# Performance work log

Hardware: AMD Instinct MI355X
Metric: run time of the kernel (lower is better)

## Reference

```python
import jax, jax.numpy as jnp
from jax import lax
import numpy as np

B, N, XS, LAT = 16, 400000, 256, 10


def setup_inputs() -> dict:
    key = jax.random.key(0)
    ks = jax.random.split(key, 9)
    flow = 2.0 * jax.random.normal(ks[0], (B, N, 3), jnp.float32)
    x = jax.random.normal(ks[1], (B, XS, XS), jnp.float32)
    values = jax.random.normal(ks[2], (N,), jnp.float32)
    # near-identity rotation matrices so most splatted points stay in-grid
    rotations = jnp.eye(3, dtype=jnp.float32)[None] + 0.05 * jax.random.normal(ks[3], (B, 3, 3), jnp.float32)
    shifts = 2.0 * jax.random.normal(ks[4], (B, 2), jnp.float32)
    w1 = 0.001 * jax.random.normal(ks[5], (XS * XS, LAT), jnp.float32)
    b1 = jnp.zeros((LAT,), jnp.float32)
    w2 = 0.1 * jax.random.normal(ks[6], (LAT, 2), jnp.float32)
    b2 = jnp.zeros((2,), jnp.float32)
    inds = jax.random.randint(ks[7], (N, 3), 0, XS, dtype=jnp.int32)
    return dict(flow=flow, x=x, values=values, rotations=rotations, shifts=shifts,
                w1=w1, b1=b1, w2=w2, b2=b2, inds=inds, xsize=XS)


def _gaussian_blur3(imgs):
    # dm_pix.gaussian_blur(sigma=1.0, kernel_size=3): separable, SAME (zero) padding
    g = jnp.exp(jnp.asarray(-0.5, imgs.dtype))
    k = jnp.stack([g, jnp.asarray(1.0, imgs.dtype), g])
    k = k / k.sum()
    xi = imgs[:, None]  # (B,1,H,W)
    kh = k.reshape(1, 1, 3, 1)
    kw = k.reshape(1, 1, 1, 3)
    xi = lax.conv_general_dilated(xi, kh, (1, 1), 'SAME')
    xi = lax.conv_general_dilated(xi, kw, (1, 1), 'SAME')
    return xi[:, 0]


def reference(flow, x, values, rotations, shifts, w1, b1, w2, b2, inds, xsize):
    factor = 0.5 * xsize
    # (1,N,3) coords in (z->x order as in source), center, deform
    coords = jnp.stack([inds[:, 2], inds[:, 1], inds[:, 0]], axis=1)[None].astype(flow.dtype)
    coords = coords - factor + flow                       # (B,N,3)
    coords = jnp.einsum('bnc,brc->bnr', coords, rotations)  # coords @ R^T
    coords = coords[..., :2] - shifts[:, None, :] + factor  # (B,N,2)
    c_sampling = jnp.stack([coords[..., 1], coords[..., 0]], axis=2)  # swap -> (row, col)

    bamp = values[None, :]                                # (1,N) broadcast over B
    bposf = jnp.floor(c_sampling)
    bposi = bposf.astype(jnp.int32)                       # (B,N,2)
    frac = c_sampling - bposf                             # fractional parts
    f0, f1 = frac[:, :, 0], frac[:, :, 1]
    a0 = bamp * (1.0 - f0) * (1.0 - f1)
    a1 = bamp * f0 * (1.0 - f1)
    a2 = bamp * f0 * f1
    a3 = bamp * (1.0 - f0) * f1
    bamp_all = jnp.concatenate([a0, a1, a2, a3], axis=1)  # (B,4N)
    bposi_all = jnp.concatenate([bposi,
                                 bposi + jnp.array((1, 0), jnp.int32),
                                 bposi + jnp.array((1, 1), jnp.int32),
                                 bposi + jnp.array((0, 1), jnp.int32)], axis=1)  # (B,4N,2)

    images = jnp.zeros((flow.shape[0], xsize, xsize), flow.dtype)

    def scatter_img(image, pos_i, amp_i):
        return image.at[pos_i[:, 0], pos_i[:, 1]].add(amp_i)

    images = jax.vmap(scatter_img)(images, bposi_all, bamp_all)
    images = _gaussian_blur3(images)

    # ImageAdjustment: per-image scalar gain/offset from conditioning image x
    h = jax.nn.relu(x.reshape(x.shape[0], -1) @ w1 + b1)
    ab = h @ w2 + b2                                      # (B,2)
    a, b = ab[:, 0], ab[:, 1]
    images = a[:, None, None] * images + b[:, None, None]
    # ctf_type == 'none' -> ctfFilter skipped
    return images
```

## Files before the change

### kernel.cpp

```cpp
#include <hip/hip_runtime.h>

#define XS     256
#define XS2    65536
#define LAT    10
#define BR     8
#define NG     (XS / BR)
#define NBINS  512
#define P1     2048
#define K_MAX  16
#define SPLIT  2
#define BINCAP 15360
#define FSCALE 262144.0f

__device__ __forceinline__ void fadd_atomic(float* p, float v) {
    unsafeAtomicAdd(p, v);
}

__device__ __forceinline__ void compute_rc(const float* __restrict__ flow,
                                           const int* __restrict__ inds,
                                           const float* __restrict__ rot,
                                           const float* __restrict__ shifts,
                                           int b, int n, int N,
                                           int& r, int& c, float& f0, float& f1) {
    const float* R = rot + b * 9;
    float r00 = R[0], r01 = R[1], r02 = R[2];
    float r10 = R[3], r11 = R[4], r12 = R[5];
    float s0 = shifts[b * 2 + 0], s1 = shifts[b * 2 + 1];
    size_t fo = ((size_t)b * N + n) * 3;
    float fw0 = flow[fo + 0], fw1 = flow[fo + 1], fw2 = flow[fo + 2];
    float v0 = (float)inds[n * 3 + 2] - 128.0f + fw0;
    float v1 = (float)inds[n * 3 + 1] - 128.0f + fw1;
    float v2 = (float)inds[n * 3 + 0] - 128.0f + fw2;
    float p0 = fmaf(v0, r00, fmaf(v1, r01, fmaf(v2, r02, 128.0f - s0)));
    float p1 = fmaf(v0, r10, fmaf(v1, r11, fmaf(v2, r12, 128.0f - s1)));
    float cs0 = p1, cs1 = p0;
    float ff0 = floorf(cs0), ff1 = floorf(cs1);
    r = (int)ff0; c = (int)ff1;
    f0 = cs0 - ff0; f1 = cs1 - ff1;
}

__device__ __forceinline__ void corner_atomic(float* I, int rr, int cc, float a) {
    if (rr >= -XS && rr < XS && cc >= -XS && cc < XS)
        fadd_atomic(I + ((rr + XS) & (XS - 1)) * XS + ((cc + XS) & (XS - 1)), a);
}

__device__ __forceinline__ bool is_fast(int r) {
    return (r >= -XS) && (r <= XS - 2) && (r != -1);
}

__device__ __forceinline__ void rec_fallback(unsigned long long rec, int bin,
                                             float* __restrict__ img) {
    unsigned w = (unsigned)rec;
    float amp = __uint_as_float((unsigned)(rec >> 32));
    int b = bin >> 5, g = bin & 31;
    int rig = w & 7, wc = (w >> 3) & 255;
    int wr = g * BR + rig;
    float f0 = (float)((w >> 13) & 511) * (1.0f / 512.0f);
    float f1 = (float)((w >> 22) & 511) * (1.0f / 512.0f);
    float g0 = 1.0f - f0, g1 = 1.0f - f1;
    float* I = img + (size_t)b * XS2;
    if (w & (1u << 11)) {
        fadd_atomic(&I[wr * XS + wc],       amp * g0 * g1);
        fadd_atomic(&I[(wr + 1) * XS + wc], amp * f0 * g1);
    }
    if (w & (1u << 12)) {
        int wc1 = (wc + 1) & 255;
        fadd_atomic(&I[wr * XS + wc1],       amp * g0 * f1);
        fadd_atomic(&I[(wr + 1) * XS + wc1], amp * f0 * f1);
    }
}

__global__ void __launch_bounds__(256)
place_direct(const float* __restrict__ flow,
             const float* __restrict__ values,
             const int* __restrict__ inds,
             const float* __restrict__ rot,
             const float* __restrict__ shifts,
             unsigned* __restrict__ gcursor,
             unsigned long long* __restrict__ recs,
             float* __restrict__ img,
             int N, int TI, int IPB) {
    __shared__ unsigned lcnt[NBINS];
    __shared__ unsigned lbase[NBINS];
    int t = threadIdx.x;
    lcnt[t] = 0; lcnt[t + 256] = 0;
    __syncthreads();

    unsigned long long rec[K_MAX];
    unsigned meta[K_MAX];
    int s = blockIdx.x * IPB;
    int e = min(s + IPB, TI);

#pragma unroll
    for (int k = 0; k < K_MAX; k++) {
        meta[k] = 0xFFFFFFFFu;
        int i = s + t + k * 256;
        if (i < e) {
            int b = i / N, n = i - b * N;
            int r, c; float f0, f1;
            compute_rc(flow, inds, rot, shifts, b, n, N, r, c, f0, f1);
            float amp = values[n];
            if (is_fast(r)) {
                int wr = (r + XS) & (XS - 1);
                int wc = c & (XS - 1);
                unsigned cv0 = (c >= -XS && c < XS) ? 1u : 0u;
                unsigned cv1 = (c + 1 >= -XS && c + 1 < XS) ? 1u : 0u;
                unsigned q0 = min(511u, (unsigned)(f0 * 512.0f + 0.5f));
                unsigned q1 = min(511u, (unsigned)(f1 * 512.0f + 0.5f));
                unsigned word = (unsigned)(wr & 7) | ((unsigned)wc << 3) |
                                (cv0 << 11) | (cv1 << 12) | (q0 << 13) | (q1 << 22);
                int bin = b * NG + (wr >> 3);
                unsigned rank = atomicAdd(&lcnt[bin], 1u);
                meta[k] = (unsigned)bin | (rank << 9);
                rec[k] = ((unsigned long long)__float_as_uint(amp) << 32) | word;
            } else {
                float g0 = 1.0f - f0, g1 = 1.0f - f1;
                float* I = img + (size_t)b * XS2;
                corner_atomic(I, r,     c,     amp * g0 * g1);
                corner_atomic(I, r + 1, c,     amp * f0 * g1);
                corner_atomic(I, r + 1, c + 1, amp * f0 * f1);
                corner_atomic(I, r,     c + 1, amp * g0 * f1);
            }
        }
    }
    __syncthreads();

    for (int bin = t; bin < NBINS; bin += 256) {
        unsigned cn = lcnt[bin];
        lbase[bin] = cn ? atomicAdd(&gcursor[bin], cn) : 0u;
    }
    __syncthreads();

#pragma unroll
    for (int k = 0; k < K_MAX; k++) {
        unsigned m = meta[k];
        if (m != 0xFFFFFFFFu) {
            unsigned bin = m & (NBINS - 1);
            unsigned idx = lbase[bin] + (m >> 9);
            if (idx < BINCAP) recs[(size_t)bin * BINCAP + idx] = rec[k];
            else rec_fallback(rec[k], (int)bin, img);
        }
    }
}

__global__ void __launch_bounds__(256)
accum_u64(const unsigned long long* __restrict__ recs,
          const unsigned* __restrict__ gcursor,
          float* __restrict__ reps,
          float* __restrict__ aprons, int B) {
    int bin = blockIdx.x / SPLIT, sp = blockIdx.x - bin * SPLIT;
    int b = bin >> 5, g = bin & 31;
    __shared__ unsigned long long tile[BR * XS];
    int t = threadIdx.x;
    for (int k = t; k < BR * XS; k += 256) tile[k] = 0ull;
    __syncthreads();

    unsigned cnt = min(gcursor[bin], (unsigned)BINCAP);
    unsigned lo = (unsigned)(((unsigned long long)cnt * sp) / SPLIT);
    unsigned hi = (unsigned)(((unsigned long long)cnt * (sp + 1)) / SPLIT);
    const unsigned long long* rb = recs + (size_t)bin * BINCAP;

    for (unsigned i = lo + t; i < hi; i += 256) {
        unsigned long long rc = rb[i];
        unsigned w = (unsigned)rc;
        float amp = __uint_as_float((unsigned)(rc >> 32));
        int rig = w & 7, wc = (w >> 3) & 255;
        float f0 = (float)((w >> 13) & 511) * (1.0f / 512.0f);
        float f1 = (float)((w >> 22) & 511) * (1.0f / 512.0f);
        float g0 = 1.0f - f0, g1 = 1.0f - f1;
        int base = rig * XS;
        if (w & (1u << 11)) {
            float cl = amp * g1;
            int qlo = __float2int_rn(cl * g0 * FSCALE);
            int qhi = __float2int_rn(cl * f0 * FSCALE);
            unsigned long long inc =
                (unsigned long long)(((long long)qhi << 32) + (long long)qlo);
            __hip_atomic_fetch_add(&tile[base + wc], inc,
                                   __ATOMIC_RELAXED, __HIP_MEMORY_SCOPE_WORKGROUP);
        }
        if (w & (1u << 12)) {
            float cr = amp * f1;
            int qlo = __float2int_rn(cr * g0 * FSCALE);
            int qhi = __float2int_rn(cr * f0 * FSCALE);
            unsigned long long inc =
                (unsigned long long)(((long long)qhi << 32) + (long long)qlo);
            __hip_atomic_fetch_add(&tile[base + ((wc + 1) & (XS - 1))], inc,
                                   __ATOMIC_RELAXED, __HIP_MEMORY_SCOPE_WORKGROUP);
        }
    }
    __syncthreads();

    const float invS = 1.0f / FSCALE;
    float* rep = reps + ((size_t)sp * B + b) * XS2;
    for (int k = t; k < (BR + 1) * XS; k += 256) {
        int row = k >> 8, col = k & 255;
        long long acc = 0;
        if (row < BR) {
            unsigned long long s0 = tile[row * XS + col];
            acc += (long long)(int)(unsigned)(s0 & 0xffffffffull);
        }
        if (row >= 1) {
            unsigned long long s1 = tile[(row - 1) * XS + col];
            long long lo32 = (long long)(int)(unsigned)(s1 & 0xffffffffull);
            acc += ((long long)s1 - lo32) >> 32;
        }
        float v = (float)acc * invS;
        if (row < BR) rep[(g * BR + row) * XS + col] = v;
        else          aprons[((size_t)bin * SPLIT + sp) * XS + col] = v;
    }
}

__global__ void combine_kernel(float* __restrict__ img,
                               const float* __restrict__ reps,
                               const float* __restrict__ aprons, int B) {
    int b = blockIdx.y, r = blockIdx.x, c = threadIdx.x;
    size_t off = (size_t)b * XS2 + r * XS + c;
    float v = img[off];
#pragma unroll
    for (int sp = 0; sp < SPLIT; sp++)
        v += reps[((size_t)sp * B + b) * XS2 + r * XS + c];
    if (r >= BR && (r & (BR - 1)) == 0) {
        int g = (r >> 3) - 1;
        int bin = b * NG + g;
#pragma unroll
        for (int sp = 0; sp < SPLIT; sp++)
            v += aprons[((size_t)bin * SPLIT + sp) * XS + c];
    }
    img[off] = v;
}

__global__ void scatter_kernel(const float* __restrict__ flow,
                               const float* __restrict__ values,
                               const int* __restrict__ inds,
                               const float* __restrict__ rot,
                               const float* __restrict__ shifts,
                               float* __restrict__ img, int N) {
    int b = blockIdx.y;
    int n = blockIdx.x * blockDim.x + threadIdx.x;
    if (n >= N) return;
    int r, c; float f0, f1;
    compute_rc(flow, inds, rot, shifts, b, n, N, r, c, f0, f1);
    float amp = values[n];
    float g0 = 1.0f - f0, g1 = 1.0f - f1;
    float* I = img + (size_t)b * XS2;
    corner_atomic(I, r,     c,     amp * g0 * g1);
    corner_atomic(I, r + 1, c,     amp * f0 * g1);
    corner_atomic(I, r + 1, c + 1, amp * f0 * f1);
    corner_atomic(I, r,     c + 1, amp * g0 * f1);
}

__global__ void mlp_partial(const float* __restrict__ x,
                            const float* __restrict__ w1,
                            float* __restrict__ hraw, int B) {
    int base = blockIdx.x * 256;
    int t = threadIdx.x;
    if (t >= B * LAT) return;
    int b = t / LAT, l = t - b * LAT;
    const float* xb = x + (size_t)b * XS2 + base;
    const float* w  = w1 + (size_t)base * LAT + l;
    float acc = 0.0f;
#pragma unroll 8
    for (int e = 0; e < 256; e++) acc += xb[e] * w[e * LAT];
    fadd_atomic(&hraw[b * LAT + l], acc);
}

__global__ void blur_kernel(const float* __restrict__ img,
                            const float* __restrict__ hraw,
                            const float* __restrict__ b1,
                            const float* __restrict__ w2,
                            const float* __restrict__ b2,
                            float* __restrict__ out) {
    int b = blockIdx.y, r = blockIdx.x, c = threadIdx.x;
    float av = b2[0], bv = b2[1];
#pragma unroll
    for (int l = 0; l < LAT; l++) {
        float h = hraw[b * LAT + l] + b1[l];
        h = h > 0.0f ? h : 0.0f;
        av += h * w2[l * 2 + 0];
        bv += h * w2[l * 2 + 1];
    }
    const float g   = 0.6065306597126334f;
    const float inv = 1.0f / (1.0f + 2.0f * g);
    const float* I = img + (size_t)b * XS2;
    float up  = (r > 0)      ? I[(r - 1) * XS + c] : 0.0f;
    float mid =                I[r * XS + c];
    float dn  = (r < XS - 1) ? I[(r + 1) * XS + c] : 0.0f;
    float v = (g * (up + dn) + mid) * inv;
    __shared__ float row[XS + 2];
    row[c + 1] = v;
    if (c == 0) { row[0] = 0.0f; row[XS + 1] = 0.0f; }
    __syncthreads();
    float hh = (g * (row[c] + row[c + 2]) + v) * inv;
    out[(size_t)b * XS2 + (size_t)r * XS + c] = av * hh + bv;
}

extern "C" void kernel_launch(void* const* d_in, const int* in_sizes, int n_in,
                              void* d_out, int out_size, void* d_ws, size_t ws_size,
                              hipStream_t stream) {
    const float* flow   = (const float*)d_in[0];
    const float* x      = (const float*)d_in[1];
    const float* values = (const float*)d_in[2];
    const float* rot    = (const float*)d_in[3];
    const float* shifts = (const float*)d_in[4];
    const float* w1     = (const float*)d_in[5];
    const float* b1     = (const float*)d_in[6];
    const float* w2     = (const float*)d_in[7];
    const float* b2     = (const float*)d_in[8];
    const int*   inds   = (const int*)d_in[9];

    int N = in_sizes[2];
    int B = in_sizes[4] / 2;
    int TI  = B * N;
    int IPB = (TI + P1 - 1) / P1;

    size_t imgElems = (size_t)B * XS2;
    float*    img     = (float*)d_ws;
    float*    hraw    = img + imgElems;
    unsigned* gcursor = (unsigned*)(hraw + 256);
    unsigned long long* recs = (unsigned long long*)(gcursor + NBINS);
    float*    reps    = (float*)(recs + (size_t)NBINS * BINCAP);
    float*    aprons  = reps + (size_t)SPLIT * imgElems;
    size_t needed = (size_t)((char*)(aprons + (size_t)NBINS * SPLIT * XS) - (char*)d_ws);

    bool fast = (B * NG == NBINS) && (ws_size >= needed) && (IPB <= K_MAX * 256);

    hipMemsetAsync(d_ws, 0, imgElems * sizeof(float) + 1024 + NBINS * 4, stream);

    if (fast) {
        place_direct<<<P1, 256, 0, stream>>>(flow, values, inds, rot, shifts,
                                             gcursor, recs, img, N, TI, IPB);
        accum_u64<<<NBINS * SPLIT, 256, 0, stream>>>(recs, gcursor, reps, aprons, B);
        dim3 gc(XS, B);
        combine_kernel<<<gc, 256, 0, stream>>>(img, reps, aprons, B);
    } else {
        dim3 g1((N + 255) / 256, B);
        scatter_kernel<<<g1, 256, 0, stream>>>(flow, values, inds, rot, shifts, img, N);
    }

    mlp_partial<<<XS2 / 256, 256, 0, stream>>>(x, w1, hraw, B);

    dim3 g3(XS, B);
    blur_kernel<<<g3, XS, 0, stream>>>(img, hraw, b1, w2, b2, (float*)d_out);
}
```

Baseline: 235.3 us.

## Replace global bin cursors with per-block scanned tables and packed 16-bit accumulation

The place kernel now does a block-local prefix scan over its bin counts and writes records into a per-block contiguous region, plus an offset table, instead of claiming slots through global atomic cursors with an overflow fallback. The accumulate kernel walks every placing block's segment for its bin and packs four 16-bit fixed-point corner contributions into one 64-bit LDS atomic over half-width cells. The separate combine kernel is removed and its sums are folded into the blur kernel's loads. This cuts global atomics, the combine pass and LDS atomic count. In exchange it uses a coarse 1/256 quantisation and 16-bit fields, which risk accuracy and overflow, and gives each accum thread long serial loops.

Result: slower. 298.2 us (+26.7%).

```diff
diff --git a/kernel.cpp b/kernel.cpp
--- a/kernel.cpp
+++ b/kernel.cpp
@@ -8,12 +8,23 @@
 #define NBINS  512
 #define P1     2048
 #define K_MAX  16
-#define SPLIT  2
-#define BINCAP 15360
-#define FSCALE 262144.0f
+#define CAP    3200
+#define TAB    513
+#define CELLW  128
+#define QS     256.0f
 
 __device__ __forceinline__ void fadd_atomic(float* p, float v) {
     unsafeAtomicAdd(p, v);
+}
+
+__device__ __forceinline__ void lds_add_u64(unsigned long long* p,
+                                            unsigned long long v) {
+    __hip_atomic_fetch_add(p, v, __ATOMIC_RELAXED, __HIP_MEMORY_SCOPE_WORKGROUP);
+}
+
+__device__ __forceinline__ unsigned long long pack4(int q0, int q1, int q2, int q3) {
+    return (unsigned long long)((long long)q0 + ((long long)q1 << 16) +
+                                ((long long)q2 << 32) + ((long long)q3 << 48));
 }
 
 __device__ __forceinline__ void compute_rc(const float* __restrict__ flow,
@@ -48,40 +59,19 @@
     return (r >= -XS) && (r <= XS - 2) && (r != -1);
 }
 
-__device__ __forceinline__ void rec_fallback(unsigned long long rec, int bin,
-                                             float* __restrict__ img) {
-    unsigned w = (unsigned)rec;
-    float amp = __uint_as_float((unsigned)(rec >> 32));
-    int b = bin >> 5, g = bin & 31;
-    int rig = w & 7, wc = (w >> 3) & 255;
-    int wr = g * BR + rig;
-    float f0 = (float)((w >> 13) & 511) * (1.0f / 512.0f);
-    float f1 = (float)((w >> 22) & 511) * (1.0f / 512.0f);
-    float g0 = 1.0f - f0, g1 = 1.0f - f1;
-    float* I = img + (size_t)b * XS2;
-    if (w & (1u << 11)) {
-        fadd_atomic(&I[wr * XS + wc],       amp * g0 * g1);
-        fadd_atomic(&I[(wr + 1) * XS + wc], amp * f0 * g1);
-    }
-    if (w & (1u << 12)) {
-        int wc1 = (wc + 1) & 255;
-        fadd_atomic(&I[wr * XS + wc1],       amp * g0 * f1);
-        fadd_atomic(&I[(wr + 1) * XS + wc1], amp * f0 * f1);
-    }
-}
-
 __global__ void __launch_bounds__(256)
-place_direct(const float* __restrict__ flow,
+place_kernel(const float* __restrict__ flow,
              const float* __restrict__ values,
              const int* __restrict__ inds,
              const float* __restrict__ rot,
              const float* __restrict__ shifts,
-             unsigned* __restrict__ gcursor,
+             unsigned* __restrict__ tab,
              unsigned long long* __restrict__ recs,
              float* __restrict__ img,
              int N, int TI, int IPB) {
     __shared__ unsigned lcnt[NBINS];
-    __shared__ unsigned lbase[NBINS];
+    __shared__ unsigned lscan[NBINS];
+    __shared__ unsigned sh[256];
     int t = threadIdx.x;
     lcnt[t] = 0; lcnt[t + 256] = 0;
     __syncthreads();
@@ -125,108 +115,98 @@
     }
     __syncthreads();
 
-    for (int bin = t; bin < NBINS; bin += 256) {
-        unsigned cn = lcnt[bin];
-        lbase[bin] = cn ? atomicAdd(&gcursor[bin], cn) : 0u;
-    }
-    __syncthreads();
-
+    unsigned v0 = lcnt[2 * t], v1 = lcnt[2 * t + 1];
+    unsigned psum = v0 + v1;
+    sh[t] = psum; __syncthreads();
+    for (int st = 1; st < 256; st <<= 1) {
+        unsigned add = (t >= st) ? sh[t - st] : 0u;
+        __syncthreads();
+        sh[t] += add;
+        __syncthreads();
+    }
+    unsigned run = sh[t] - psum;
+    lscan[2 * t] = run;
+    lscan[2 * t + 1] = run + v0;
+    __syncthreads();
+
+    unsigned* tb = tab + (size_t)blockIdx.x * TAB;
+    tb[t] = lscan[t];
+    tb[t + 256] = lscan[t + 256];
+    if (t == 0) tb[512] = sh[255];
+
+    unsigned long long* rb = recs + (size_t)blockIdx.x * CAP;
 #pragma unroll
     for (int k = 0; k < K_MAX; k++) {
         unsigned m = meta[k];
         if (m != 0xFFFFFFFFu) {
             unsigned bin = m & (NBINS - 1);
-            unsigned idx = lbase[bin] + (m >> 9);
-            if (idx < BINCAP) recs[(size_t)bin * BINCAP + idx] = rec[k];
-            else rec_fallback(rec[k], (int)bin, img);
+            rb[lscan[bin] + (m >> 9)] = rec[k];
         }
     }
 }
 
 __global__ void __launch_bounds__(256)
-accum_u64(const unsigned long long* __restrict__ recs,
-          const unsigned* __restrict__ gcursor,
-          float* __restrict__ reps,
-          float* __restrict__ aprons, int B) {
-    int bin = blockIdx.x / SPLIT, sp = blockIdx.x - bin * SPLIT;
+accum_kernel(const unsigned long long* __restrict__ recs,
+             const unsigned* __restrict__ tab,
+             float* __restrict__ reps,
+             float* __restrict__ aprons, int B) {
+    int bin = blockIdx.x >> 1, sp = blockIdx.x & 1;
     int b = bin >> 5, g = bin & 31;
-    __shared__ unsigned long long tile[BR * XS];
+    __shared__ unsigned long long tile[BR * CELLW];
     int t = threadIdx.x;
-    for (int k = t; k < BR * XS; k += 256) tile[k] = 0ull;
-    __syncthreads();
-
-    unsigned cnt = min(gcursor[bin], (unsigned)BINCAP);
-    unsigned lo = (unsigned)(((unsigned long long)cnt * sp) / SPLIT);
-    unsigned hi = (unsigned)(((unsigned long long)cnt * (sp + 1)) / SPLIT);
-    const unsigned long long* rb = recs + (size_t)bin * BINCAP;
-
-    for (unsigned i = lo + t; i < hi; i += 256) {
-        unsigned long long rc = rb[i];
-        unsigned w = (unsigned)rc;
-        float amp = __uint_as_float((unsigned)(rc >> 32));
-        int rig = w & 7, wc = (w >> 3) & 255;
-        float f0 = (float)((w >> 13) & 511) * (1.0f / 512.0f);
-        float f1 = (float)((w >> 22) & 511) * (1.0f / 512.0f);
-        float g0 = 1.0f - f0, g1 = 1.0f - f1;
-        int base = rig * XS;
-        if (w & (1u << 11)) {
-            float cl = amp * g1;
-            int qlo = __float2int_rn(cl * g0 * FSCALE);
-            int qhi = __float2int_rn(cl * f0 * FSCALE);
-            unsigned long long inc =
-                (unsigned long long)(((long long)qhi << 32) + (long long)qlo);
-            __hip_atomic_fetch_add(&tile[base + wc], inc,
-                                   __ATOMIC_RELAXED, __HIP_MEMORY_SCOPE_WORKGROUP);
+    for (int k = t; k < BR * CELLW; k += 256) tile[k] = 0ull;
+    __syncthreads();
+
+#pragma unroll
+    for (int q = 0; q < P1 / 512; q++) {
+        int blk = sp + 2 * (q * 256 + t);
+        const unsigned* tb = tab + (size_t)blk * TAB + bin;
+        unsigned o = tb[0], e2 = tb[1];
+        const unsigned long long* rb = recs + (size_t)blk * CAP;
+        for (unsigned i = o; i < e2; i++) {
+            unsigned long long rc = rb[i];
+            unsigned w = (unsigned)rc;
+            float amp = __uint_as_float((unsigned)(rc >> 32));
+            int rig = w & 7, wc = (w >> 3) & 255;
+            float f0 = (float)((w >> 13) & 511) * (1.0f / 512.0f);
+            float f1 = (float)((w >> 22) & 511) * (1.0f / 512.0f);
+            float g0 = 1.0f - f0, g1 = 1.0f - f1;
+            bool cv0 = (w >> 11) & 1, cv1 = (w >> 12) & 1;
+            int base = rig * CELLW;
+            int i00 = __float2int_rn(amp * g0 * g1 * QS);
+            int i10 = __float2int_rn(amp * f0 * g1 * QS);
+            int i01 = __float2int_rn(amp * g0 * f1 * QS);
+            int i11 = __float2int_rn(amp * f0 * f1 * QS);
+            if ((wc & 1) == 0) {
+                unsigned long long inc = pack4(cv0 ? i00 : 0, cv0 ? i10 : 0,
+                                               cv1 ? i01 : 0, cv1 ? i11 : 0);
+                if (inc) lds_add_u64(&tile[base + (wc >> 1)], inc);
+            } else {
+                if (cv0) lds_add_u64(&tile[base + (wc >> 1)], pack4(0, 0, i00, i10));
+                if (cv1) lds_add_u64(&tile[base + (((wc + 1) & 255) >> 1)],
+                                     pack4(i01, i11, 0, 0));
+            }
         }
-        if (w & (1u << 12)) {
-            float cr = amp * f1;
-            int qlo = __float2int_rn(cr * g0 * FSCALE);
-            int qhi = __float2int_rn(cr * f0 * FSCALE);
-            unsigned long long inc =
-                (unsigned long long)(((long long)qhi << 32) + (long long)qlo);
-            __hip_atomic_fetch_add(&tile[base + ((wc + 1) & (XS - 1))], inc,
-                                   __ATOMIC_RELAXED, __HIP_MEMORY_SCOPE_WORKGROUP);
-        }
-    }
-    __syncthreads();
-
-    const float invS = 1.0f / FSCALE;
+    }
+    __syncthreads();
+
+    int c = t, j = c >> 1, p = c & 1;
+    const float invS = 1.0f / QS;
     float* rep = reps + ((size_t)sp * B + b) * XS2;
-    for (int k = t; k < (BR + 1) * XS; k += 256) {
-        int row = k >> 8, col = k & 255;
-        long long acc = 0;
-        if (row < BR) {
-            unsigned long long s0 = tile[row * XS + col];
-            acc += (long long)(int)(unsigned)(s0 & 0xffffffffull);
-        }
-        if (row >= 1) {
-            unsigned long long s1 = tile[(row - 1) * XS + col];
-            long long lo32 = (long long)(int)(unsigned)(s1 & 0xffffffffull);
-            acc += ((long long)s1 - lo32) >> 32;
-        }
-        float v = (float)acc * invS;
-        if (row < BR) rep[(g * BR + row) * XS + col] = v;
-        else          aprons[((size_t)bin * SPLIT + sp) * XS + col] = v;
-    }
-}
-
-__global__ void combine_kernel(float* __restrict__ img,
-                               const float* __restrict__ reps,
-                               const float* __restrict__ aprons, int B) {
-    int b = blockIdx.y, r = blockIdx.x, c = threadIdx.x;
-    size_t off = (size_t)b * XS2 + r * XS + c;
-    float v = img[off];
-#pragma unroll
-    for (int sp = 0; sp < SPLIT; sp++)
-        v += reps[((size_t)sp * B + b) * XS2 + r * XS + c];
-    if (r >= BR && (r & (BR - 1)) == 0) {
-        int g = (r >> 3) - 1;
-        int bin = b * NG + g;
-#pragma unroll
-        for (int sp = 0; sp < SPLIT; sp++)
-            v += aprons[((size_t)bin * SPLIT + sp) * XS + c];
-    }
-    img[off] = v;
+    float carry = 0.0f;
+#pragma unroll
+    for (int rig = 0; rig < BR; rig++) {
+        long long s = (long long)tile[rig * CELLW + j];
+        int q0 = (int)(short)(s & 0xffff); s = (s - q0) >> 16;
+        int q1 = (int)(short)(s & 0xffff); s = (s - q1) >> 16;
+        int q2 = (int)(short)(s & 0xffff); s = (s - q2) >> 16;
+        int q3 = (int)s;
+        float r0 = p ? (float)q2 : (float)q0;
+        float r1 = p ? (float)q3 : (float)q1;
+        rep[(g * BR + rig) * XS + c] = (carry + r0) * invS;
+        carry = r1;
+    }
+    aprons[((size_t)bin * 2 + sp) * XS + c] = carry * invS;
 }
 
 __global__ void scatter_kernel(const float* __restrict__ flow,
@@ -264,12 +244,30 @@
     fadd_atomic(&hraw[b * LAT + l], acc);
 }
 
+__device__ __forceinline__ float S_load(const float* __restrict__ img,
+                                        const float* __restrict__ reps,
+                                        const float* __restrict__ aprons,
+                                        int B, int b, int row, int c, int fast) {
+    size_t o = (size_t)b * XS2 + row * XS + c;
+    float v = img[o];
+    if (fast) {
+        v += reps[o] + reps[(size_t)B * XS2 + o];
+        if (row > 0 && (row & 7) == 0) {
+            size_t bin = (size_t)b * NG + ((row >> 3) - 1);
+            v += aprons[bin * 2 * XS + c] + aprons[(bin * 2 + 1) * XS + c];
+        }
+    }
+    return v;
+}
+
 __global__ void blur_kernel(const float* __restrict__ img,
+                            const float* __restrict__ reps,
+                            const float* __restrict__ aprons,
                             const float* __restrict__ hraw,
                             const float* __restrict__ b1,
                             const float* __restrict__ w2,
                             const float* __restrict__ b2,
-                            float* __restrict__ out) {
+                            float* __restrict__ out, int B, int fast) {
     int b = blockIdx.y, r = blockIdx.x, c = threadIdx.x;
     float av = b2[0], bv = b2[1];
 #pragma unroll
@@ -281,10 +279,9 @@
     }
     const float g   = 0.6065306597126334f;
     const float inv = 1.0f / (1.0f + 2.0f * g);
-    const float* I = img + (size_t)b * XS2;
-    float up  = (r > 0)      ? I[(r - 1) * XS + c] : 0.0f;
-    float mid =                I[r * XS + c];
-    float dn  = (r < XS - 1) ? I[(r + 1) * XS + c] : 0.0f;
+    float up  = (r > 0)      ? S_load(img, reps, aprons, B, b, r - 1, c, fast) : 0.0f;
+    float mid =                S_load(img, reps, aprons, B, b, r,     c, fast);
+    float dn  = (r < XS - 1) ? S_load(img, reps, aprons, B, b, r + 1, c, fast) : 0.0f;
     float v = (g * (up + dn) + mid) * inv;
     __shared__ float row[XS + 2];
     row[c + 1] = v;
@@ -314,24 +311,23 @@
     int IPB = (TI + P1 - 1) / P1;
 
     size_t imgElems = (size_t)B * XS2;
-    float*    img     = (float*)d_ws;
-    float*    hraw    = img + imgElems;
-    unsigned* gcursor = (unsigned*)(hraw + 256);
-    unsigned long long* recs = (unsigned long long*)(gcursor + NBINS);
-    float*    reps    = (float*)(recs + (size_t)NBINS * BINCAP);
-    float*    aprons  = reps + (size_t)SPLIT * imgElems;
-    size_t needed = (size_t)((char*)(aprons + (size_t)NBINS * SPLIT * XS) - (char*)d_ws);
-
-    bool fast = (B * NG == NBINS) && (ws_size >= needed) && (IPB <= K_MAX * 256);
-
-    hipMemsetAsync(d_ws, 0, imgElems * sizeof(float) + 1024 + NBINS * 4, stream);
+    float*    img   = (float*)d_ws;
+    float*    hraw  = img + imgElems;
+    unsigned long long* recs = (unsigned long long*)(hraw + 256);
+    unsigned* tabp  = (unsigned*)(recs + (size_t)P1 * CAP);
+    float*    reps  = (float*)(tabp + (size_t)P1 * TAB + 2);
+    float*    aprons = reps + 2 * imgElems;
+    size_t needed = (size_t)((char*)(aprons + (size_t)NBINS * 2 * XS) - (char*)d_ws);
+
+    bool fast = (B * NG == NBINS) && (ws_size >= needed) &&
+                (IPB <= CAP) && (IPB <= K_MAX * 256);
+
+    hipMemsetAsync(d_ws, 0, (imgElems + 256) * sizeof(float), stream);
 
     if (fast) {
-        place_direct<<<P1, 256, 0, stream>>>(flow, values, inds, rot, shifts,
-                                             gcursor, recs, img, N, TI, IPB);
-        accum_u64<<<NBINS * SPLIT, 256, 0, stream>>>(recs, gcursor, reps, aprons, B);
-        dim3 gc(XS, B);
-        combine_kernel<<<gc, 256, 0, stream>>>(img, reps, aprons, B);
+        place_kernel<<<P1, 256, 0, stream>>>(flow, values, inds, rot, shifts,
+                                             tabp, recs, img, N, TI, IPB);
+        accum_kernel<<<NBINS * 2, 256, 0, stream>>>(recs, tabp, reps, aprons, B);
     } else {
         dim3 g1((N + 255) / 256, B);
         scatter_kernel<<<g1, 256, 0, stream>>>(flow, values, inds, rot, shifts, img, N);
@@ -340,5 +336,6 @@
     mlp_partial<<<XS2 / 256, 256, 0, stream>>>(x, w1, hraw, B);
 
     dim3 g3(XS, B);
-    blur_kernel<<<g3, XS, 0, stream>>>(img, hraw, b1, w2, b2, (float*)d_out);
-}
+    blur_kernel<<<g3, XS, 0, stream>>>(img, reps, aprons, hraw, b1, w2, b2,
+                                       (float*)d_out, B, fast ? 1 : 0);
+}
```

## Pack four bilinear corners into one 16-bit-lane LDS atomic and fuse combine into blur

Applied to the files above, without the earlier changes.

The accumulation kernel now quantizes all four bilinear corner weights to 16-bit lanes and adds them with a single 64-bit LDS atomic per record. Columns are split into even and odd tiles, and lanes are unpacked with carry handling in the epilogue. The separate combine kernel is removed: the blur kernel sums the image, both replicas and the apron rows when it loads. The placement grid and per-thread record count are also retuned. Risks: the coarser quantization scale (1/256) lowers accuracy, and the blur does three times as many global loads.

After: 221.1 us. 6.0% less time.

```diff
diff --git a/kernel.cpp b/kernel.cpp
--- a/kernel.cpp
+++ b/kernel.cpp
@@ -6,14 +6,25 @@
 #define BR     8
 #define NG     (XS / BR)
 #define NBINS  512
-#define P1     2048
-#define K_MAX  16
+#define P1     1024
+#define K_MAX  25
+#define BINCAP 15360
 #define SPLIT  2
-#define BINCAP 15360
-#define FSCALE 262144.0f
+#define CELLW  128
+#define QS     256.0f
 
 __device__ __forceinline__ void fadd_atomic(float* p, float v) {
     unsafeAtomicAdd(p, v);
+}
+
+__device__ __forceinline__ void lds_add_u64(unsigned long long* p,
+                                            unsigned long long v) {
+    __hip_atomic_fetch_add(p, v, __ATOMIC_RELAXED, __HIP_MEMORY_SCOPE_WORKGROUP);
+}
+
+__device__ __forceinline__ unsigned long long pack4(int q0, int q1, int q2, int q3) {
+    return (unsigned long long)((long long)q0 + ((long long)q1 << 16) +
+                                ((long long)q2 << 32) + ((long long)q3 << 48));
 }
 
 __device__ __forceinline__ void compute_rc(const float* __restrict__ flow,
@@ -71,7 +82,7 @@
 }
 
 __global__ void __launch_bounds__(256)
-place_direct(const float* __restrict__ flow,
+place_kernel(const float* __restrict__ flow,
              const float* __restrict__ values,
              const int* __restrict__ inds,
              const float* __restrict__ rot,
@@ -144,15 +155,16 @@
 }
 
 __global__ void __launch_bounds__(256)
-accum_u64(const unsigned long long* __restrict__ recs,
-          const unsigned* __restrict__ gcursor,
-          float* __restrict__ reps,
-          float* __restrict__ aprons, int B) {
-    int bin = blockIdx.x / SPLIT, sp = blockIdx.x - bin * SPLIT;
+accum_kernel(const unsigned long long* __restrict__ recs,
+             const unsigned* __restrict__ gcursor,
+             float* __restrict__ reps,
+             float* __restrict__ aprons, int B) {
+    int bin = blockIdx.x >> 1, sp = blockIdx.x & 1;
     int b = bin >> 5, g = bin & 31;
-    __shared__ unsigned long long tile[BR * XS];
+    __shared__ unsigned long long teven[BR * CELLW];
+    __shared__ unsigned long long todd[BR * CELLW];
     int t = threadIdx.x;
-    for (int k = t; k < BR * XS; k += 256) tile[k] = 0ull;
+    for (int k = t; k < BR * CELLW; k += 256) { teven[k] = 0ull; todd[k] = 0ull; }
     __syncthreads();
 
     unsigned cnt = min(gcursor[bin], (unsigned)BINCAP);
@@ -168,65 +180,43 @@
         float f0 = (float)((w >> 13) & 511) * (1.0f / 512.0f);
         float f1 = (float)((w >> 22) & 511) * (1.0f / 512.0f);
         float g0 = 1.0f - f0, g1 = 1.0f - f1;
-        int base = rig * XS;
-        if (w & (1u << 11)) {
-            float cl = amp * g1;
-            int qlo = __float2int_rn(cl * g0 * FSCALE);
-            int qhi = __float2int_rn(cl * f0 * FSCALE);
-            unsigned long long inc =
-                (unsigned long long)(((long long)qhi << 32) + (long long)qlo);
-            __hip_atomic_fetch_add(&tile[base + wc], inc,
-                                   __ATOMIC_RELAXED, __HIP_MEMORY_SCOPE_WORKGROUP);
-        }
-        if (w & (1u << 12)) {
-            float cr = amp * f1;
-            int qlo = __float2int_rn(cr * g0 * FSCALE);
-            int qhi = __float2int_rn(cr * f0 * FSCALE);
-            unsigned long long inc =
-                (unsigned long long)(((long long)qhi << 32) + (long long)qlo);
-            __hip_atomic_fetch_add(&tile[base + ((wc + 1) & (XS - 1))], inc,
-                                   __ATOMIC_RELAXED, __HIP_MEMORY_SCOPE_WORKGROUP);
-        }
-    }
-    __syncthreads();
-
-    const float invS = 1.0f / FSCALE;
+        bool cv0 = (w >> 11) & 1, cv1 = (w >> 12) & 1;
+        int q00 = cv0 ? __float2int_rn(amp * g0 * g1 * QS) : 0;
+        int q10 = cv0 ? __float2int_rn(amp * f0 * g1 * QS) : 0;
+        int q01 = cv1 ? __float2int_rn(amp * g0 * f1 * QS) : 0;
+        int q11 = cv1 ? __float2int_rn(amp * f0 * f1 * QS) : 0;
+        unsigned long long inc = pack4(q00, q10, q01, q11);
+        unsigned long long* tile = (wc & 1) ? todd : teven;
+        if (inc) lds_add_u64(&tile[rig * CELLW + (wc >> 1)], inc);
+    }
+    __syncthreads();
+
+    int c = t;
+    int je = c >> 1;
+    int jo = (c & 1) ? (c >> 1) : (((c + 254) & 255) >> 1);
+    bool e_lo = (c & 1) == 0;
+    bool o_lo = (c & 1) == 1;
+    const float invS = 1.0f / QS;
     float* rep = reps + ((size_t)sp * B + b) * XS2;
-    for (int k = t; k < (BR + 1) * XS; k += 256) {
-        int row = k >> 8, col = k & 255;
-        long long acc = 0;
-        if (row < BR) {
-            unsigned long long s0 = tile[row * XS + col];
-            acc += (long long)(int)(unsigned)(s0 & 0xffffffffull);
-        }
-        if (row >= 1) {
-            unsigned long long s1 = tile[(row - 1) * XS + col];
-            long long lo32 = (long long)(int)(unsigned)(s1 & 0xffffffffull);
-            acc += ((long long)s1 - lo32) >> 32;
-        }
-        float v = (float)acc * invS;
-        if (row < BR) rep[(g * BR + row) * XS + col] = v;
-        else          aprons[((size_t)bin * SPLIT + sp) * XS + col] = v;
-    }
-}
-
-__global__ void combine_kernel(float* __restrict__ img,
-                               const float* __restrict__ reps,
-                               const float* __restrict__ aprons, int B) {
-    int b = blockIdx.y, r = blockIdx.x, c = threadIdx.x;
-    size_t off = (size_t)b * XS2 + r * XS + c;
-    float v = img[off];
+    float carry = 0.0f;
 #pragma unroll
-    for (int sp = 0; sp < SPLIT; sp++)
-        v += reps[((size_t)sp * B + b) * XS2 + r * XS + c];
-    if (r >= BR && (r & (BR - 1)) == 0) {
-        int g = (r >> 3) - 1;
-        int bin = b * NG + g;
-#pragma unroll
-        for (int sp = 0; sp < SPLIT; sp++)
-            v += aprons[((size_t)bin * SPLIT + sp) * XS + c];
-    }
-    img[off] = v;
+    for (int rig = 0; rig < BR; rig++) {
+        long long se = (long long)teven[rig * CELLW + je];
+        int e0 = (int)(short)(se & 0xffff); se = (se - e0) >> 16;
+        int e1 = (int)(short)(se & 0xffff); se = (se - e1) >> 16;
+        int e2 = (int)(short)(se & 0xffff); se = (se - e2) >> 16;
+        int e3 = (int)se;
+        long long so = (long long)todd[rig * CELLW + jo];
+        int o0 = (int)(short)(so & 0xffff); so = (so - o0) >> 16;
+        int o1 = (int)(short)(so & 0xffff); so = (so - o1) >> 16;
+        int o2 = (int)(short)(so & 0xffff); so = (so - o2) >> 16;
+        int o3 = (int)so;
+        float r0 = (e_lo ? (float)e0 : (float)e2) + (o_lo ? (float)o0 : (float)o2);
+        float r1 = (e_lo ? (float)e1 : (float)e3) + (o_lo ? (float)o1 : (float)o3);
+        rep[(g * BR + rig) * XS + c] = (carry + r0) * invS;
+        carry = r1;
+    }
+    aprons[((size_t)bin * 2 + sp) * XS + c] = carry * invS;
 }
 
 __global__ void scatter_kernel(const float* __restrict__ flow,
@@ -264,12 +254,30 @@
     fadd_atomic(&hraw[b * LAT + l], acc);
 }
 
+__device__ __forceinline__ float S_load(const float* __restrict__ img,
+                                        const float* __restrict__ reps,
+                                        const float* __restrict__ aprons,
+                                        int B, int b, int row, int c, int fast) {
+    size_t o = (size_t)b * XS2 + row * XS + c;
+    float v = img[o];
+    if (fast) {
+        v += reps[o] + reps[(size_t)B * XS2 + o];
+        if (row > 0 && (row & 7) == 0) {
+            size_t bin = (size_t)b * NG + ((row >> 3) - 1);
+            v += aprons[bin * 2 * XS + c] + aprons[(bin * 2 + 1) * XS + c];
+        }
+    }
+    return v;
+}
+
 __global__ void blur_kernel(const float* __restrict__ img,
+                            const float* __restrict__ reps,
+                            const float* __restrict__ aprons,
                             const float* __restrict__ hraw,
                             const float* __restrict__ b1,
                             const float* __restrict__ w2,
                             const float* __restrict__ b2,
-                            float* __restrict__ out) {
+                            float* __restrict__ out, int B, int fast) {
     int b = blockIdx.y, r = blockIdx.x, c = threadIdx.x;
     float av = b2[0], bv = b2[1];
 #pragma unroll
@@ -281,10 +289,9 @@
     }
     const float g   = 0.6065306597126334f;
     const float inv = 1.0f / (1.0f + 2.0f * g);
-    const float* I = img + (size_t)b * XS2;
-    float up  = (r > 0)      ? I[(r - 1) * XS + c] : 0.0f;
-    float mid =                I[r * XS + c];
-    float dn  = (r < XS - 1) ? I[(r + 1) * XS + c] : 0.0f;
+    float up  = (r > 0)      ? S_load(img, reps, aprons, B, b, r - 1, c, fast) : 0.0f;
+    float mid =                S_load(img, reps, aprons, B, b, r,     c, fast);
+    float dn  = (r < XS - 1) ? S_load(img, reps, aprons, B, b, r + 1, c, fast) : 0.0f;
     float v = (g * (up + dn) + mid) * inv;
     __shared__ float row[XS + 2];
     row[c + 1] = v;
@@ -319,19 +326,17 @@
     unsigned* gcursor = (unsigned*)(hraw + 256);
     unsigned long long* recs = (unsigned long long*)(gcursor + NBINS);
     float*    reps    = (float*)(recs + (size_t)NBINS * BINCAP);
-    float*    aprons  = reps + (size_t)SPLIT * imgElems;
-    size_t needed = (size_t)((char*)(aprons + (size_t)NBINS * SPLIT * XS) - (char*)d_ws);
+    float*    aprons  = reps + 2 * imgElems;
+    size_t needed = (size_t)((char*)(aprons + (size_t)NBINS * 2 * XS) - (char*)d_ws);
 
     bool fast = (B * NG == NBINS) && (ws_size >= needed) && (IPB <= K_MAX * 256);
 
     hipMemsetAsync(d_ws, 0, imgElems * sizeof(float) + 1024 + NBINS * 4, stream);
 
     if (fast) {
-        place_direct<<<P1, 256, 0, stream>>>(flow, values, inds, rot, shifts,
+        place_kernel<<<P1, 256, 0, stream>>>(flow, values, inds, rot, shifts,
                                              gcursor, recs, img, N, TI, IPB);
-        accum_u64<<<NBINS * SPLIT, 256, 0, stream>>>(recs, gcursor, reps, aprons, B);
-        dim3 gc(XS, B);
-        combine_kernel<<<gc, 256, 0, stream>>>(img, reps, aprons, B);
+        accum_kernel<<<NBINS * SPLIT, 256, 0, stream>>>(recs, gcursor, reps, aprons, B);
     } else {
         dim3 g1((N + 255) / 256, B);
         scatter_kernel<<<g1, 256, 0, stream>>>(flow, values, inds, rot, shifts, img, N);
@@ -340,5 +345,6 @@
     mlp_partial<<<XS2 / 256, 256, 0, stream>>>(x, w1, hraw, B);
 
     dim3 g3(XS, B);
-    blur_kernel<<<g3, XS, 0, stream>>>(img, hraw, b1, w2, b2, (float*)d_out);
-}
+    blur_kernel<<<g3, XS, 0, stream>>>(img, reps, aprons, hraw, b1, w2, b2,
+                                       (float*)d_out, B, fast ? 1 : 0);
+}
```
